# Performance work log

Hardware: AMD Instinct MI355X
Metric: run time of the kernel (lower is better)

Reference implementation:

```python
import jax, jax.numpy as jnp
import numpy as np

N_NODES = 100000


def gcn_conv(x, W, b, src, dst, n_nodes):
    # Linear transform first (PyG GCNConv applies weight before propagation)
    h = x @ W  # [N, out]
    # gcn_norm with self-loops: deg[i] = 1 + #incoming edges at i
    ones = jnp.ones(src.shape[0], dtype=h.dtype)
    deg = jax.ops.segment_sum(ones, dst, num_segments=n_nodes) + 1.0
    dinv = jax.lax.rsqrt(deg)  # deg^{-1/2}, deg >= 1 so safe
    norm = dinv[src] * dinv[dst]  # [E]
    # aggregate normalized messages at destination nodes
    agg = jax.ops.segment_sum(h[src] * norm[:, None], dst, num_segments=n_nodes)
    # self-loop contribution: norm_ii = dinv[i]^2
    agg = agg + h * (dinv * dinv)[:, None]
    return agg + b


def setup_inputs() -> dict:
    key = jax.random.key(0)
    k1, k2, k3, k4, k5, k6 = jax.random.split(key, 6)
    num_features, hidden, num_classes = 512, 128, 64
    x = jax.random.normal(k1, (N_NODES, num_features), dtype=jnp.float32)
    edge_index = jax.random.randint(k2, (2, 1600000), 0, N_NODES, dtype=jnp.int64)
    # Glorot-style params (scaled normals)
    W1 = jax.random.normal(k3, (num_features, hidden), dtype=jnp.float32) / np.sqrt(num_features)
    b1 = jnp.zeros((hidden,), dtype=jnp.float32)
    W2 = jax.random.normal(k4, (hidden, num_classes), dtype=jnp.float32) / np.sqrt(hidden)
    b2 = jnp.zeros((num_classes,), dtype=jnp.float32)
    return {"x": x, "edge_index": edge_index, "W1": W1, "b1": b1, "W2": W2, "b2": b2}


def reference(x, edge_index, W1, b1, W2, b2):
    src, dst = edge_index[0], edge_index[1]
    h = jax.nn.relu(gcn_conv(x, W1, b1, src, dst, N_NODES))
    out = gcn_conv(h, W2, b2, src, dst, N_NODES)
    return jax.nn.log_softmax(out, axis=1)
```

## Files before the change

### kernel.cpp

```cpp
#include <hip/hip_runtime.h>
#include <cmath>

#define N_NODES 100000
#define N_EDGES 1600000
#define F_IN 512
#define F_HID 128
#define F_OUT 64

#define SCAN_NB ((N_NODES + 255) / 256)

#define BK_SHIFT 10
#define NBUK ((N_NODES + 1023) >> 10)
#define SCAP 24576
#define LSLOT 64
#define NBLK_A 512
#define FILL_SPLIT 8
#define NPS (1024 / FILL_SPLIT)
#define OV_CAP 4096

typedef __attribute__((ext_vector_type(8))) short short8;
typedef __attribute__((ext_vector_type(4))) float float4v;

#define GLOAD_LDS16(g, l)                                                      \
    __builtin_amdgcn_global_load_lds(                                          \
        (const __attribute__((address_space(1))) void*)(g),                    \
        (__attribute__((address_space(3))) void*)(l), 16, 0, 0)

__device__ __forceinline__ unsigned short f2bf(float f) {
    unsigned u = __builtin_bit_cast(unsigned, f);
    u += 0x7FFFu + ((u >> 16) & 1u);
    return (unsigned short)(u >> 16);
}
__device__ __forceinline__ float bf2f(unsigned short s) {
    unsigned u = ((unsigned)s) << 16;
    return __builtin_bit_cast(float, u);
}
__device__ __forceinline__ float lo_bf(unsigned u) {
    return __builtin_bit_cast(float, u << 16);
}
__device__ __forceinline__ float hi_bf(unsigned u) {
    return __builtin_bit_cast(float, u & 0xFFFF0000u);
}
__device__ __forceinline__ short8 cvt8(float4 lo, float4 hi) {
    return short8{(short)f2bf(lo.x), (short)f2bf(lo.y), (short)f2bf(lo.z), (short)f2bf(lo.w),
                  (short)f2bf(hi.x), (short)f2bf(hi.y), (short)f2bf(hi.z), (short)f2bf(hi.w)};
}
__device__ __forceinline__ unsigned pack_bf2(float a, float b) {
    return (unsigned)f2bf(a) | ((unsigned)f2bf(b) << 16);
}

template <int N>
__device__ __forceinline__ void waitvm() {
    if constexpr (N == 0) asm volatile("s_waitcnt vmcnt(0)" ::: "memory");
    else if constexpr (N == 3) asm volatile("s_waitcnt vmcnt(3)" ::: "memory");
    else if constexpr (N == 6) asm volatile("s_waitcnt vmcnt(6)" ::: "memory");
    else static_assert(N == 0 || N == 3 || N == 6, "add literal");
}
#define LGKM0() asm volatile("s_waitcnt lgkmcnt(0)" ::: "memory")
#define BAR() __builtin_amdgcn_s_barrier()
#define SCHED0() __builtin_amdgcn_sched_barrier(0)

__global__ __launch_bounds__(256) void partition_kernel(
    const int* __restrict__ src, const int* __restrict__ dst,
    int* __restrict__ deg, unsigned* __restrict__ staging, int* __restrict__ gcur,
    unsigned long long* __restrict__ ovbuf, int* __restrict__ ovcnt) {
    __shared__ unsigned buf[NBUK][LSLOT];
    __shared__ int cnt[NBUK];
    int tid = threadIdx.x;
    for (int b = tid; b < NBUK; b += 256) cnt[b] = 0;
    __syncthreads();
    constexpr int PER = (((N_EDGES + NBLK_A - 1) / NBLK_A) + 3) & ~3;
    int e0 = blockIdx.x * PER;
    int e1 = min(e0 + PER, N_EDGES);

    auto body = [&](int d, int s) {
        atomicAdd(&deg[d], 1);
        int b = d >> BK_SHIFT;
        unsigned rec = (unsigned)s | ((unsigned)(d & 1023) << 17);
        int slot = atomicAdd(&cnt[b], 1);
        if (slot < LSLOT) {
            buf[b][slot] = rec;
        } else {
            int op = atomicAdd(ovcnt, 1);
            if (op < OV_CAP)
                ovbuf[op] = ((unsigned long long)(unsigned)d << 32) | (unsigned)s;
        }
    };
    auto drain = [&](void) {
        for (int b = tid; b < NBUK; b += 256) {
            int c = min(cnt[b], LSLOT);
            int full = c & ~15;
            if (full > 0) {
                int pos = atomicAdd(&gcur[b], full);
                if (pos + full <= SCAP) {
                    unsigned* dp = &staging[(size_t)b * SCAP + pos];
                    for (int i = 0; i < full; ++i) dp[i] = buf[b][i];
                }
                for (int i = 0; i < c - full; ++i) buf[b][i] = buf[b][full + i];
            }
            cnt[b] = c - full;
        }
    };

    int base = e0;
    for (; base + 1024 <= e1; base += 1024) {
        int e = base + tid * 4;
        int4 dv = *(const int4*)(dst + e);
        int4 sv = *(const int4*)(src + e);
        body(dv.x, sv.x);
        body(dv.y, sv.y);
        body(dv.z, sv.z);
        body(dv.w, sv.w);
        __syncthreads();
        drain();
        __syncthreads();
    }
    for (int e = base + tid; e < e1; e += 256) body(dst[e], src[e]);
    __syncthreads();
    drain();
    __syncthreads();
    for (int b = tid; b < NBUK; b += 256) {
        int c = cnt[b];
        if (c > 0) {
            int pos = atomicAdd(&gcur[b], c);
            if (pos + c <= SCAP)
                for (int i = 0; i < c; ++i) staging[(size_t)b * SCAP + pos + i] = buf[b][i];
        }
    }
}

__global__ __launch_bounds__(256) void fill_kernel(
    const unsigned* __restrict__ staging, const int* __restrict__ gcur,
    const int* __restrict__ row_ptr, int* __restrict__ csr_src,
    const unsigned long long* __restrict__ ovbuf, const int* __restrict__ ovcnt) {
    int b = blockIdx.x / FILL_SPLIT;
    int slice = blockIdx.x - b * FILL_SPLIT;
    int dl0 = slice * NPS;
    int node0 = (b << BK_SHIFT) + dl0;
    __shared__ int lcur[NPS];
    int tid = threadIdx.x;
    if (tid < NPS) {
        int nd = node0 + tid;
        lcur[tid] = (nd < N_NODES) ? row_ptr[nd] : 0;
    }
    __syncthreads();

    int n = gcur[b];
    if (n > SCAP) n = SCAP;
    const unsigned* sp = &staging[(size_t)b * SCAP];

    auto process = [&](unsigned rec) {
        int dl = (int)(rec >> 17) - dl0;
        if ((unsigned)dl < (unsigned)NPS) {
            int pos = atomicAdd(&lcur[dl], 1);
            csr_src[pos] = (int)(rec & 0x1FFFFu);
        }
    };

    int i = tid * 4;
    for (; i + 4 <= n; i += 1024) {
        uint4 r = *(const uint4*)(sp + i);
        process(r.x);
        process(r.y);
        process(r.z);
        process(r.w);
    }
    int tail0 = n & ~3;
    if (tid < (n - tail0)) process(sp[tail0 + tid]);

    int oc = *ovcnt;
    if (oc > OV_CAP) oc = OV_CAP;
    for (int k = tid; k < oc; k += 256) {
        unsigned long long r = ovbuf[k];
        int d = (int)(r >> 32);
        int dl = d - node0;
        if ((d >> BK_SHIFT) == b && (unsigned)dl < (unsigned)NPS) {
            int pos = atomicAdd(&lcur[dl], 1);
            csr_src[pos] = (int)(r & 0xffffffffu);
        }
    }
}


__global__ __launch_bounds__(256) void block_sum_kernel(const int* __restrict__ deg,
                                                        int* __restrict__ bsum, int n) {
    int g = blockIdx.x * 256 + threadIdx.x;
    int v = (g < n) ? deg[g] : 0;
    __shared__ int ws[4];
    int lane = threadIdx.x & 63;
    int w = threadIdx.x >> 6;
#pragma unroll
    for (int o = 32; o > 0; o >>= 1) v += __shfl_down(v, o, 64);
    if (lane == 0) ws[w] = v;
    __syncthreads();
    if (threadIdx.x == 0) bsum[blockIdx.x] = ws[0] + ws[1] + ws[2] + ws[3];
}

__global__ __launch_bounds__(512) void scan_partials_kernel(int* __restrict__ bsum, int nb) {
    __shared__ int t[512];
    int tid = threadIdx.x;
    int v = (tid < nb) ? bsum[tid] : 0;
    t[tid] = v;
    __syncthreads();
    for (int d = 1; d < 512; d <<= 1) {
        int u = (tid >= d) ? t[tid - d] : 0;
        __syncthreads();
        t[tid] += u;
        __syncthreads();
    }
    if (tid < nb) bsum[tid] = t[tid] - v;
}

__global__ __launch_bounds__(256) void scan_final_kernel(const int* __restrict__ deg,
                                                         const int* __restrict__ bsum,
                                                         int* __restrict__ row_ptr,
                                                         float* __restrict__ dinv, int n) {
    __shared__ int t[256];
    int g = blockIdx.x * 256 + threadIdx.x;
    int tid = threadIdx.x;
    int v = (g < n) ? deg[g] : 0;
    t[tid] = v;
    __syncthreads();
    for (int d = 1; d < 256; d <<= 1) {
        int u = (tid >= d) ? t[tid - d] : 0;
        __syncthreads();
        t[tid] += u;
        __syncthreads();
    }
    int off = bsum[blockIdx.x] + t[tid] - v;
    if (g < n) {
        row_ptr[g] = off;
        dinv[g] = rsqrtf((float)(v + 1));
    }
    if (g == n - 1) row_ptr[n] = off + v;
}


__global__ void transpose_w_kernel(const float* __restrict__ W1, const float* __restrict__ W2,
                                   unsigned short* __restrict__ Wt1,
                                   unsigned short* __restrict__ Wt2) {
    int g = blockIdx.x * 256 + threadIdx.x;
    if (g < F_HID * F_IN) {
        int n = g >> 9, k = g & 511;
        Wt1[g] = f2bf(W1[k * F_HID + n]);
    } else {
        int h = g - F_HID * F_IN;
        if (h < F_OUT * F_HID) {
            int n = h >> 7, k = h & 127;
            Wt2[h] = f2bf(W2[k * F_OUT + n]);
        }
    }
}


template <int BN, int K, bool A_BF16>
__global__ __launch_bounds__(256, 3) void gemm_lds_kernel(
    const void* __restrict__ Araw, const unsigned short* __restrict__ Wt,
    const float* __restrict__ dinv, unsigned short* __restrict__ out, int N) {
    constexpr int NCT = BN / 16;
    constexpr int AE = A_BF16 ? 2 : 4;
    constexpr int SLOTS_A = (32 * AE) / 16;
    constexpr int MA = SLOTS_A - 1;
    constexpr int ABYTES = 128 * 32 * AE;
    constexpr int BBYTES = BN * 32 * 2;
    constexpr int NT = K / 32;
    constexpr int SL = (128 * SLOTS_A + BN * 4) / 256;

    __shared__ __align__(128) char Abuf[2][ABYTES];
    __shared__ __align__(128) char Bbuf[2][BBYTES];

    const char* Ab = (const char*)Araw;
    const char* Bb = (const char*)Wt;
    int tid = threadIdx.x;
    int lane = tid & 63;
    int wv = tid >> 6;
    int row0 = blockIdx.x * 128;
    int l15 = lane & 15;
    int q = lane >> 4;

    float4v acc[2][NCT] = {};

    auto stage = [&](int buf, int k0) {
        constexpr int CA = 128 * SLOTS_A;
#pragma unroll
        for (int i = 0; i < CA / 256; ++i) {
            int c = i * 256 + tid;
            int cw = i * 256 + (tid & ~63);
            int row = c / SLOTS_A;
            int s = c & MA;
            int g = s ^ (row & MA);
            int rg = row0 + row;
            if (rg >= N) rg = N - 1;
            GLOAD_LDS16(Ab + ((size_t)rg * K + k0) * AE + g * 16,
                        &Abuf[buf][cw * 16]);
        }
        constexpr int CB = BN * 4;
#pragma unroll
        for (int i = 0; i < CB / 256; ++i) {
            int c = i * 256 + tid;
            int cw = i * 256 + (tid & ~63);
            int col = c >> 2;
            int s = c & 3;
            int g = s ^ (col & 3);
            GLOAD_LDS16(Bb + ((size_t)col * K + k0) * 2 + g * 16,
                        &Bbuf[buf][cw * 16]);
        }
    };

    auto compute = [&](int buf) {
        const char* Ac = Abuf[buf];
        const char* Bc = Bbuf[buf];
        int lr0 = wv * 32 + l15;
        int lr1 = lr0 + 16;
        short8 a0, a1;
        if constexpr (A_BF16) {
            int s0 = q ^ (lr0 & 3);
            int s1 = q ^ (lr1 & 3);
            a0 = *(const short8*)(Ac + lr0 * 64 + s0 * 16);
            a1 = *(const short8*)(Ac + lr1 * 64 + s1 * 16);
        } else {
            int r7a = lr0 & 7, r7b = lr1 & 7;
            float4 f0 = *(const float4*)(Ac + lr0 * 128 + ((2 * q) ^ r7a) * 16);
            float4 f1 = *(const float4*)(Ac + lr0 * 128 + ((2 * q + 1) ^ r7a) * 16);
            float4 f2 = *(const float4*)(Ac + lr1 * 128 + ((2 * q) ^ r7b) * 16);
            float4 f3 = *(const float4*)(Ac + lr1 * 128 + ((2 * q + 1) ^ r7b) * 16);
            a0 = cvt8(f0, f1);
            a1 = cvt8(f2, f3);
        }
#pragma unroll
        for (int ct = 0; ct < NCT; ++ct) {
            int col = ct * 16 + l15;
            int sb = q ^ (col & 3);
            short8 b = *(const short8*)(Bc + col * 64 + sb * 16);
            acc[0][ct] = __builtin_amdgcn_mfma_f32_16x16x32_bf16(a0, b, acc[0][ct], 0, 0, 0);
            acc[1][ct] = __builtin_amdgcn_mfma_f32_16x16x32_bf16(a1, b, acc[1][ct], 0, 0, 0);
        }
    };

    stage(0, 0);
    stage(1, 32);
#pragma unroll 1
    for (int t = 0; t < NT - 2; ++t) {
        waitvm<SL>();
        BAR();
        SCHED0();
        compute(t & 1);
        LGKM0();
        BAR();
        SCHED0();
        stage(t & 1, (t + 2) * 32);
    }
    waitvm<SL>();
    BAR();
    SCHED0();
    compute((NT - 2) & 1);
    waitvm<0>();
    BAR();
    SCHED0();
    compute((NT - 1) & 1);

#pragma unroll
    for (int rt = 0; rt < 2; ++rt) {
#pragma unroll
        for (int reg = 0; reg < 4; ++reg) {
            int row = row0 + wv * 32 + rt * 16 + q * 4 + reg;
            if (row < N) {
                float sc = dinv[row];
#pragma unroll
                for (int ct = 0; ct < NCT; ++ct) {
                    out[(size_t)row * BN + ct * 16 + l15] = f2bf(acc[rt][ct][reg] * sc);
                }
            }
        }
    }
}


__global__ __launch_bounds__(256) void agg1_kernel(
    const uint2* __restrict__ g1v, const int* __restrict__ row_ptr,
    const int* __restrict__ csr_src, const float* __restrict__ dinv,
    const float4* __restrict__ b1v, uint2* __restrict__ h1v) {
    int tid = threadIdx.x;
    int wv = tid >> 6;
    int lane = tid & 63;
    int half = lane >> 5;
    int hl = lane & 31;
    int node = blockIdx.x * 8 + wv * 2 + half;
    uint2 u = g1v[(size_t)node * 32 + hl];
    float a0 = lo_bf(u.x), a1 = hi_bf(u.x), a2 = lo_bf(u.y), a3 = hi_bf(u.y);
    int e = row_ptr[node], end = row_ptr[node + 1];
    for (; e + 8 <= end; e += 8) {
        int j0 = csr_src[e + 0], j1 = csr_src[e + 1], j2 = csr_src[e + 2], j3 = csr_src[e + 3];
        int j4 = csr_src[e + 4], j5 = csr_src[e + 5], j6 = csr_src[e + 6], j7 = csr_src[e + 7];
        uint2 v0 = g1v[(size_t)j0 * 32 + hl];
        uint2 v1 = g1v[(size_t)j1 * 32 + hl];
        uint2 v2 = g1v[(size_t)j2 * 32 + hl];
        uint2 v3 = g1v[(size_t)j3 * 32 + hl];
        uint2 v4 = g1v[(size_t)j4 * 32 + hl];
        uint2 v5 = g1v[(size_t)j5 * 32 + hl];
        uint2 v6 = g1v[(size_t)j6 * 32 + hl];
        uint2 v7 = g1v[(size_t)j7 * 32 + hl];
        a0 += ((lo_bf(v0.x) + lo_bf(v1.x)) + (lo_bf(v2.x) + lo_bf(v3.x))) +
              ((lo_bf(v4.x) + lo_bf(v5.x)) + (lo_bf(v6.x) + lo_bf(v7.x)));
        a1 += ((hi_bf(v0.x) + hi_bf(v1.x)) + (hi_bf(v2.x) + hi_bf(v3.x))) +
              ((hi_bf(v4.x) + hi_bf(v5.x)) + (hi_bf(v6.x) + hi_bf(v7.x)));
        a2 += ((lo_bf(v0.y) + lo_bf(v1.y)) + (lo_bf(v2.y) + lo_bf(v3.y))) +
              ((lo_bf(v4.y) + lo_bf(v5.y)) + (lo_bf(v6.y) + lo_bf(v7.y)));
        a3 += ((hi_bf(v0.y) + hi_bf(v1.y)) + (hi_bf(v2.y) + hi_bf(v3.y))) +
              ((hi_bf(v4.y) + hi_bf(v5.y)) + (hi_bf(v6.y) + hi_bf(v7.y)));
    }
    for (; e + 2 <= end; e += 2) {
        int j0 = csr_src[e + 0], j1 = csr_src[e + 1];
        uint2 v0 = g1v[(size_t)j0 * 32 + hl];
        uint2 v1 = g1v[(size_t)j1 * 32 + hl];
        a0 += lo_bf(v0.x) + lo_bf(v1.x);
        a1 += hi_bf(v0.x) + hi_bf(v1.x);
        a2 += lo_bf(v0.y) + lo_bf(v1.y);
        a3 += hi_bf(v0.y) + hi_bf(v1.y);
    }
    for (; e < end; ++e) {
        uint2 v0 = g1v[(size_t)csr_src[e] * 32 + hl];
        a0 += lo_bf(v0.x);
        a1 += hi_bf(v0.x);
        a2 += lo_bf(v0.y);
        a3 += hi_bf(v0.y);
    }
    float d = dinv[node];
    float4 b = b1v[hl];
    float r0 = fmaxf(d * a0 + b.x, 0.0f);
    float r1 = fmaxf(d * a1 + b.y, 0.0f);
    float r2 = fmaxf(d * a2 + b.z, 0.0f);
    float r3 = fmaxf(d * a3 + b.w, 0.0f);
    h1v[(size_t)node * 32 + hl] = uint2{pack_bf2(r0, r1), pack_bf2(r2, r3)};
}

__global__ __launch_bounds__(256) void agg2_lsm_kernel(
    const unsigned* __restrict__ g2v, const int* __restrict__ row_ptr,
    const int* __restrict__ csr_src, const float* __restrict__ dinv,
    const float2* __restrict__ b2v, float2* __restrict__ outv) {
    int tid = threadIdx.x;
    int wv = tid >> 6;
    int lane = tid & 63;
    int half = lane >> 5;
    int hl = lane & 31;
    int node = blockIdx.x * 8 + wv * 2 + half;
    unsigned u = g2v[(size_t)node * 32 + hl];
    float a0 = lo_bf(u), a1 = hi_bf(u);
    int e = row_ptr[node], end = row_ptr[node + 1];
    for (; e + 8 <= end; e += 8) {
        int j0 = csr_src[e + 0], j1 = csr_src[e + 1], j2 = csr_src[e + 2], j3 = csr_src[e + 3];
        int j4 = csr_src[e + 4], j5 = csr_src[e + 5], j6 = csr_src[e + 6], j7 = csr_src[e + 7];
        unsigned v0 = g2v[(size_t)j0 * 32 + hl];
        unsigned v1 = g2v[(size_t)j1 * 32 + hl];
        unsigned v2 = g2v[(size_t)j2 * 32 + hl];
        unsigned v3 = g2v[(size_t)j3 * 32 + hl];
        unsigned v4 = g2v[(size_t)j4 * 32 + hl];
        unsigned v5 = g2v[(size_t)j5 * 32 + hl];
        unsigned v6 = g2v[(size_t)j6 * 32 + hl];
        unsigned v7 = g2v[(size_t)j7 * 32 + hl];
        a0 += ((lo_bf(v0) + lo_bf(v1)) + (lo_bf(v2) + lo_bf(v3))) +
              ((lo_bf(v4) + lo_bf(v5)) + (lo_bf(v6) + lo_bf(v7)));
        a1 += ((hi_bf(v0) + hi_bf(v1)) + (hi_bf(v2) + hi_bf(v3))) +
              ((hi_bf(v4) + hi_bf(v5)) + (hi_bf(v6) + hi_bf(v7)));
    }
    for (; e + 2 <= end; e += 2) {
        unsigned v0 = g2v[(size_t)csr_src[e + 0] * 32 + hl];
        unsigned v1 = g2v[(size_t)csr_src[e + 1] * 32 + hl];
        a0 += lo_bf(v0) + lo_bf(v1);
        a1 += hi_bf(v0) + hi_bf(v1);
    }
    for (; e < end; ++e) {
        unsigned v0 = g2v[(size_t)csr_src[e] * 32 + hl];
        a0 += lo_bf(v0);
        a1 += hi_bf(v0);
    }
    float d = dinv[node];
    float2 b = b2v[hl];
    float v0 = d * a0 + b.x;
    float v1 = d * a1 + b.y;
    float m = fmaxf(v0, v1);
#pragma unroll
    for (int o = 16; o > 0; o >>= 1) m = fmaxf(m, __shfl_xor(m, o, 64));
    float s = __expf(v0 - m) + __expf(v1 - m);
#pragma unroll
    for (int o = 16; o > 0; o >>= 1) s += __shfl_xor(s, o, 64);
    float ls = __logf(s);
    outv[(size_t)node * 32 + hl] = float2{v0 - m - ls, v1 - m - ls};
}


extern "C" void kernel_launch(void* const* d_in, const int* in_sizes, int n_in,
                              void* d_out, int out_size, void* d_ws, size_t ws_size,
                              hipStream_t stream) {
    const float* x  = (const float*)d_in[0];
    const int* eidx = (const int*)d_in[1];
    const float* W1 = (const float*)d_in[2];
    const float* b1 = (const float*)d_in[3];
    const float* W2 = (const float*)d_in[4];
    const float* b2 = (const float*)d_in[5];
    float* out = (float*)d_out;
    const int* src = eidx;
    const int* dst = eidx + N_EDGES;

    char* base = (char*)d_ws;
    size_t off = 0;
    auto alloc = [&](size_t bytes) -> void* {
        void* p = base + off;
        off += (bytes + 255) & ~(size_t)255;
        return p;
    };
    int* zbase    = (int*)alloc((size_t)(N_NODES + NBUK + 64) * 4);
    int* deg      = zbase;
    int* gcur     = zbase + N_NODES;
    int* ovcnt    = zbase + N_NODES + NBUK;
    int* row_ptr  = (int*)alloc((size_t)(N_NODES + 1) * 4);
    float* dinv   = (float*)alloc((size_t)N_NODES * 4);
    int* bsum     = (int*)alloc((size_t)SCAN_NB * 4);
    unsigned* staging = (unsigned*)alloc((size_t)NBUK * SCAP * 4);
    unsigned long long* ovbuf = (unsigned long long*)alloc((size_t)OV_CAP * 8);
    int* csr_src  = (int*)alloc((size_t)N_EDGES * 4);
    unsigned short* Wt1 = (unsigned short*)alloc((size_t)F_HID * F_IN * 2);
    unsigned short* Wt2 = (unsigned short*)alloc((size_t)F_OUT * F_HID * 2);
    unsigned short* g1  = (unsigned short*)alloc((size_t)N_NODES * F_HID * 2);
    unsigned short* h1  = (unsigned short*)alloc((size_t)N_NODES * F_HID * 2);
    unsigned short* g2  = g1;

    hipMemsetAsync(zbase, 0, (size_t)(N_NODES + NBUK + 64) * 4, stream);
    partition_kernel<<<NBLK_A, 256, 0, stream>>>(src, dst, deg, staging, gcur, ovbuf, ovcnt);
    block_sum_kernel<<<SCAN_NB, 256, 0, stream>>>(deg, bsum, N_NODES);
    scan_partials_kernel<<<1, 512, 0, stream>>>(bsum, SCAN_NB);
    scan_final_kernel<<<SCAN_NB, 256, 0, stream>>>(deg, bsum, row_ptr, dinv, N_NODES);
    fill_kernel<<<NBUK * FILL_SPLIT, 256, 0, stream>>>(staging, gcur, row_ptr, csr_src, ovbuf, ovcnt);
    transpose_w_kernel<<<(F_HID * F_IN + F_OUT * F_HID + 255) / 256, 256, 0, stream>>>(
        W1, W2, Wt1, Wt2);

    int gblocks = (N_NODES + 127) / 128;
    gemm_lds_kernel<F_HID, F_IN, false><<<gblocks, 256, 0, stream>>>(
        (const void*)x, Wt1, dinv, g1, N_NODES);
    agg1_kernel<<<N_NODES / 8, 256, 0, stream>>>(
        (const uint2*)g1, row_ptr, csr_src, dinv, (const float4*)b1, (uint2*)h1);

    gemm_lds_kernel<F_OUT, F_HID, true><<<gblocks, 256, 0, stream>>>(
        (const void*)h1, Wt2, dinv, g2, N_NODES);
    agg2_lsm_kernel<<<N_NODES / 8, 256, 0, stream>>>(
        (const unsigned*)g2, row_ptr, csr_src, dinv, (const float2*)b2, (float2*)out);
}
```

Before: 557.5 us.

## Compute degrees via per-bucket LDS histogram and widen aggregation gathers to 16B

Removes the global atomicAdd on deg for every edge in the partition kernel. Degrees are now computed by a new per-bucket kernel that builds an LDS histogram from the staged records and the overflow buffer. Both aggregation kernels now use quarter-wave groups (16 lanes per node) with wider vector loads, uint4 for layer 1 and uint2 for layer 2, so each gather issues fewer, larger memory transactions and the log-softmax reduction needs fewer shuffles. This adds one kernel launch and an extra pass over the staging buffer, and each lane now holds more accumulators.

```diff
diff --git a/kernel.cpp b/kernel.cpp
--- a/kernel.cpp
+++ b/kernel.cpp
@@ -62,7 +62,7 @@
 
 __global__ __launch_bounds__(256) void partition_kernel(
     const int* __restrict__ src, const int* __restrict__ dst,
-    int* __restrict__ deg, unsigned* __restrict__ staging, int* __restrict__ gcur,
+    unsigned* __restrict__ staging, int* __restrict__ gcur,
     unsigned long long* __restrict__ ovbuf, int* __restrict__ ovcnt) {
     __shared__ unsigned buf[NBUK][LSLOT];
     __shared__ int cnt[NBUK];
@@ -74,7 +74,6 @@
     int e1 = min(e0 + PER, N_EDGES);
 
     auto body = [&](int d, int s) {
-        atomicAdd(&deg[d], 1);
         int b = d >> BK_SHIFT;
         unsigned rec = (unsigned)s | ((unsigned)(d & 1023) << 17);
         int slot = atomicAdd(&cnt[b], 1);
@@ -126,6 +125,42 @@
             if (pos + c <= SCAP)
                 for (int i = 0; i < c; ++i) staging[(size_t)b * SCAP + pos + i] = buf[b][i];
         }
+    }
+}
+
+__global__ __launch_bounds__(256) void deg_hist_kernel(
+    const unsigned* __restrict__ staging, const int* __restrict__ gcur,
+    const unsigned long long* __restrict__ ovbuf, const int* __restrict__ ovcnt,
+    int* __restrict__ deg) {
+    int b = blockIdx.x;
+    __shared__ int hist[1024];
+    int tid = threadIdx.x;
+    for (int i = tid; i < 1024; i += 256) hist[i] = 0;
+    __syncthreads();
+    int n = gcur[b];
+    if (n > SCAP) n = SCAP;
+    const unsigned* sp = &staging[(size_t)b * SCAP];
+    int i = tid * 4;
+    for (; i + 4 <= n; i += 1024) {
+        uint4 r = *(const uint4*)(sp + i);
+        atomicAdd(&hist[r.x >> 17], 1);
+        atomicAdd(&hist[r.y >> 17], 1);
+        atomicAdd(&hist[r.z >> 17], 1);
+        atomicAdd(&hist[r.w >> 17], 1);
+    }
+    int tail0 = n & ~3;
+    if (tid < (n - tail0)) atomicAdd(&hist[sp[tail0 + tid] >> 17], 1);
+    int oc = *ovcnt;
+    if (oc > OV_CAP) oc = OV_CAP;
+    for (int k = tid; k < oc; k += 256) {
+        int d = (int)(ovbuf[k] >> 32);
+        if ((d >> BK_SHIFT) == b) atomicAdd(&hist[d & 1023], 1);
+    }
+    __syncthreads();
+    int node0 = b << BK_SHIFT;
+    for (int j = tid; j < 1024; j += 256) {
+        int nd = node0 + j;
+        if (nd < N_NODES) deg[nd] = hist[j];
     }
 }
 
@@ -377,115 +412,109 @@
 
 
 __global__ __launch_bounds__(256) void agg1_kernel(
-    const uint2* __restrict__ g1v, const int* __restrict__ row_ptr,
+    const uint4* __restrict__ g1v, const int* __restrict__ row_ptr,
     const int* __restrict__ csr_src, const float* __restrict__ dinv,
-    const float4* __restrict__ b1v, uint2* __restrict__ h1v) {
+    const float4* __restrict__ b1v, uint4* __restrict__ h1v) {
     int tid = threadIdx.x;
     int wv = tid >> 6;
     int lane = tid & 63;
-    int half = lane >> 5;
-    int hl = lane & 31;
-    int node = blockIdx.x * 8 + wv * 2 + half;
-    uint2 u = g1v[(size_t)node * 32 + hl];
+    int qt = lane >> 4;
+    int ql = lane & 15;
+    int node = blockIdx.x * 16 + wv * 4 + qt;
+    uint4 u = g1v[(size_t)node * 16 + ql];
     float a0 = lo_bf(u.x), a1 = hi_bf(u.x), a2 = lo_bf(u.y), a3 = hi_bf(u.y);
+    float a4 = lo_bf(u.z), a5 = hi_bf(u.z), a6 = lo_bf(u.w), a7 = hi_bf(u.w);
     int e = row_ptr[node], end = row_ptr[node + 1];
+#define ACC8(v)                                                                \
+    a0 += lo_bf(v.x); a1 += hi_bf(v.x); a2 += lo_bf(v.y); a3 += hi_bf(v.y);    \
+    a4 += lo_bf(v.z); a5 += hi_bf(v.z); a6 += lo_bf(v.w); a7 += hi_bf(v.w)
     for (; e + 8 <= end; e += 8) {
         int j0 = csr_src[e + 0], j1 = csr_src[e + 1], j2 = csr_src[e + 2], j3 = csr_src[e + 3];
         int j4 = csr_src[e + 4], j5 = csr_src[e + 5], j6 = csr_src[e + 6], j7 = csr_src[e + 7];
-        uint2 v0 = g1v[(size_t)j0 * 32 + hl];
-        uint2 v1 = g1v[(size_t)j1 * 32 + hl];
-        uint2 v2 = g1v[(size_t)j2 * 32 + hl];
-        uint2 v3 = g1v[(size_t)j3 * 32 + hl];
-        uint2 v4 = g1v[(size_t)j4 * 32 + hl];
-        uint2 v5 = g1v[(size_t)j5 * 32 + hl];
-        uint2 v6 = g1v[(size_t)j6 * 32 + hl];
-        uint2 v7 = g1v[(size_t)j7 * 32 + hl];
-        a0 += ((lo_bf(v0.x) + lo_bf(v1.x)) + (lo_bf(v2.x) + lo_bf(v3.x))) +
-              ((lo_bf(v4.x) + lo_bf(v5.x)) + (lo_bf(v6.x) + lo_bf(v7.x)));
-        a1 += ((hi_bf(v0.x) + hi_bf(v1.x)) + (hi_bf(v2.x) + hi_bf(v3.x))) +
-              ((hi_bf(v4.x) + hi_bf(v5.x)) + (hi_bf(v6.x) + hi_bf(v7.x)));
-        a2 += ((lo_bf(v0.y) + lo_bf(v1.y)) + (lo_bf(v2.y) + lo_bf(v3.y))) +
-              ((lo_bf(v4.y) + lo_bf(v5.y)) + (lo_bf(v6.y) + lo_bf(v7.y)));
-        a3 += ((hi_bf(v0.y) + hi_bf(v1.y)) + (hi_bf(v2.y) + hi_bf(v3.y))) +
-              ((hi_bf(v4.y) + hi_bf(v5.y)) + (hi_bf(v6.y) + hi_bf(v7.y)));
+        uint4 v0 = g1v[(size_t)j0 * 16 + ql];
+        uint4 v1 = g1v[(size_t)j1 * 16 + ql];
+        uint4 v2 = g1v[(size_t)j2 * 16 + ql];
+        uint4 v3 = g1v[(size_t)j3 * 16 + ql];
+        uint4 v4 = g1v[(size_t)j4 * 16 + ql];
+        uint4 v5 = g1v[(size_t)j5 * 16 + ql];
+        uint4 v6 = g1v[(size_t)j6 * 16 + ql];
+        uint4 v7 = g1v[(size_t)j7 * 16 + ql];
+        ACC8(v0); ACC8(v1); ACC8(v2); ACC8(v3);
+        ACC8(v4); ACC8(v5); ACC8(v6); ACC8(v7);
     }
     for (; e + 2 <= end; e += 2) {
-        int j0 = csr_src[e + 0], j1 = csr_src[e + 1];
-        uint2 v0 = g1v[(size_t)j0 * 32 + hl];
-        uint2 v1 = g1v[(size_t)j1 * 32 + hl];
-        a0 += lo_bf(v0.x) + lo_bf(v1.x);
-        a1 += hi_bf(v0.x) + hi_bf(v1.x);
-        a2 += lo_bf(v0.y) + lo_bf(v1.y);
-        a3 += hi_bf(v0.y) + hi_bf(v1.y);
+        uint4 v0 = g1v[(size_t)csr_src[e + 0] * 16 + ql];
+        uint4 v1 = g1v[(size_t)csr_src[e + 1] * 16 + ql];
+        ACC8(v0); ACC8(v1);
     }
     for (; e < end; ++e) {
-        uint2 v0 = g1v[(size_t)csr_src[e] * 32 + hl];
-        a0 += lo_bf(v0.x);
-        a1 += hi_bf(v0.x);
-        a2 += lo_bf(v0.y);
-        a3 += hi_bf(v0.y);
-    }
+        uint4 v0 = g1v[(size_t)csr_src[e] * 16 + ql];
+        ACC8(v0);
+    }
+#undef ACC8
     float d = dinv[node];
-    float4 b = b1v[hl];
-    float r0 = fmaxf(d * a0 + b.x, 0.0f);
-    float r1 = fmaxf(d * a1 + b.y, 0.0f);
-    float r2 = fmaxf(d * a2 + b.z, 0.0f);
-    float r3 = fmaxf(d * a3 + b.w, 0.0f);
-    h1v[(size_t)node * 32 + hl] = uint2{pack_bf2(r0, r1), pack_bf2(r2, r3)};
+    float4 ba = b1v[2 * ql], bb = b1v[2 * ql + 1];
+    float r0 = fmaxf(d * a0 + ba.x, 0.0f), r1 = fmaxf(d * a1 + ba.y, 0.0f);
+    float r2 = fmaxf(d * a2 + ba.z, 0.0f), r3 = fmaxf(d * a3 + ba.w, 0.0f);
+    float r4 = fmaxf(d * a4 + bb.x, 0.0f), r5 = fmaxf(d * a5 + bb.y, 0.0f);
+    float r6 = fmaxf(d * a6 + bb.z, 0.0f), r7 = fmaxf(d * a7 + bb.w, 0.0f);
+    h1v[(size_t)node * 16 + ql] =
+        uint4{pack_bf2(r0, r1), pack_bf2(r2, r3), pack_bf2(r4, r5), pack_bf2(r6, r7)};
 }
 
 __global__ __launch_bounds__(256) void agg2_lsm_kernel(
-    const unsigned* __restrict__ g2v, const int* __restrict__ row_ptr,
+    const uint2* __restrict__ g2v, const int* __restrict__ row_ptr,
     const int* __restrict__ csr_src, const float* __restrict__ dinv,
-    const float2* __restrict__ b2v, float2* __restrict__ outv) {
+    const float4* __restrict__ b2v, float4* __restrict__ outv) {
     int tid = threadIdx.x;
     int wv = tid >> 6;
     int lane = tid & 63;
-    int half = lane >> 5;
-    int hl = lane & 31;
-    int node = blockIdx.x * 8 + wv * 2 + half;
-    unsigned u = g2v[(size_t)node * 32 + hl];
-    float a0 = lo_bf(u), a1 = hi_bf(u);
+    int qt = lane >> 4;
+    int ql = lane & 15;
+    int node = blockIdx.x * 16 + wv * 4 + qt;
+    uint2 u = g2v[(size_t)node * 16 + ql];
+    float a0 = lo_bf(u.x), a1 = hi_bf(u.x), a2 = lo_bf(u.y), a3 = hi_bf(u.y);
     int e = row_ptr[node], end = row_ptr[node + 1];
+#define ACC4(v)                                                                \
+    a0 += lo_bf(v.x); a1 += hi_bf(v.x); a2 += lo_bf(v.y); a3 += hi_bf(v.y)
     for (; e + 8 <= end; e += 8) {
         int j0 = csr_src[e + 0], j1 = csr_src[e + 1], j2 = csr_src[e + 2], j3 = csr_src[e + 3];
         int j4 = csr_src[e + 4], j5 = csr_src[e + 5], j6 = csr_src[e + 6], j7 = csr_src[e + 7];
-        unsigned v0 = g2v[(size_t)j0 * 32 + hl];
-        unsigned v1 = g2v[(size_t)j1 * 32 + hl];
-        unsigned v2 = g2v[(size_t)j2 * 32 + hl];
-        unsigned v3 = g2v[(size_t)j3 * 32 + hl];
-        unsigned v4 = g2v[(size_t)j4 * 32 + hl];
-        unsigned v5 = g2v[(size_t)j5 * 32 + hl];
-        unsigned v6 = g2v[(size_t)j6 * 32 + hl];
-        unsigned v7 = g2v[(size_t)j7 * 32 + hl];
-        a0 += ((lo_bf(v0) + lo_bf(v1)) + (lo_bf(v2) + lo_bf(v3))) +
-              ((lo_bf(v4) + lo_bf(v5)) + (lo_bf(v6) + lo_bf(v7)));
-        a1 += ((hi_bf(v0) + hi_bf(v1)) + (hi_bf(v2) + hi_bf(v3))) +
-              ((hi_bf(v4) + hi_bf(v5)) + (hi_bf(v6) + hi_bf(v7)));
+        uint2 v0 = g2v[(size_t)j0 * 16 + ql];
+        uint2 v1 = g2v[(size_t)j1 * 16 + ql];
+        uint2 v2 = g2v[(size_t)j2 * 16 + ql];
+        uint2 v3 = g2v[(size_t)j3 * 16 + ql];
+        uint2 v4 = g2v[(size_t)j4 * 16 + ql];
+        uint2 v5 = g2v[(size_t)j5 * 16 + ql];
+        uint2 v6 = g2v[(size_t)j6 * 16 + ql];
+        uint2 v7 = g2v[(size_t)j7 * 16 + ql];
+        ACC4(v0); ACC4(v1); ACC4(v2); ACC4(v3);
+        ACC4(v4); ACC4(v5); ACC4(v6); ACC4(v7);
     }
     for (; e + 2 <= end; e += 2) {
-        unsigned v0 = g2v[(size_t)csr_src[e + 0] * 32 + hl];
-        unsigned v1 = g2v[(size_t)csr_src[e + 1] * 32 + hl];
-        a0 += lo_bf(v0) + lo_bf(v1);
-        a1 += hi_bf(v0) + hi_bf(v1);
+        uint2 v0 = g2v[(size_t)csr_src[e + 0] * 16 + ql];
+        uint2 v1 = g2v[(size_t)csr_src[e + 1] * 16 + ql];
+        ACC4(v0); ACC4(v1);
     }
     for (; e < end; ++e) {
-        unsigned v0 = g2v[(size_t)csr_src[e] * 32 + hl];
-        a0 += lo_bf(v0);
-        a1 += hi_bf(v0);
-    }
+        uint2 v0 = g2v[(size_t)csr_src[e] * 16 + ql];
+        ACC4(v0);
+    }
+#undef ACC4
     float d = dinv[node];
-    float2 b = b2v[hl];
+    float4 b = b2v[ql];
     float v0 = d * a0 + b.x;
     float v1 = d * a1 + b.y;
-    float m = fmaxf(v0, v1);
-#pragma unroll
-    for (int o = 16; o > 0; o >>= 1) m = fmaxf(m, __shfl_xor(m, o, 64));
-    float s = __expf(v0 - m) + __expf(v1 - m);
-#pragma unroll
-    for (int o = 16; o > 0; o >>= 1) s += __shfl_xor(s, o, 64);
-    float ls = __logf(s);
-    outv[(size_t)node * 32 + hl] = float2{v0 - m - ls, v1 - m - ls};
+    float v2 = d * a2 + b.z;
+    float v3 = d * a3 + b.w;
+    float m = fmaxf(fmaxf(v0, v1), fmaxf(v2, v3));
+#pragma unroll
+    for (int o = 8; o > 0; o >>= 1) m = fmaxf(m, __shfl_xor(m, o, 64));
+    float s = __expf(v0 - m) + __expf(v1 - m) + __expf(v2 - m) + __expf(v3 - m);
+#pragma unroll
+    for (int o = 8; o > 0; o >>= 1) s += __shfl_xor(s, o, 64);
+    float ls = m + __logf(s);
+    outv[(size_t)node * 16 + ql] = float4{v0 - ls, v1 - ls, v2 - ls, v3 - ls};
 }
 
 
@@ -509,10 +538,10 @@
         off += (bytes + 255) & ~(size_t)255;
         return p;
     };
-    int* zbase    = (int*)alloc((size_t)(N_NODES + NBUK + 64) * 4);
-    int* deg      = zbase;
-    int* gcur     = zbase + N_NODES;
-    int* ovcnt    = zbase + N_NODES + NBUK;
+    int* zbase    = (int*)alloc((size_t)(NBUK + 64) * 4);
+    int* gcur     = zbase;
+    int* ovcnt    = zbase + NBUK;
+    int* deg      = (int*)alloc((size_t)N_NODES * 4);
     int* row_ptr  = (int*)alloc((size_t)(N_NODES + 1) * 4);
     float* dinv   = (float*)alloc((size_t)N_NODES * 4);
     int* bsum     = (int*)alloc((size_t)SCAN_NB * 4);
@@ -525,8 +554,9 @@
     unsigned short* h1  = (unsigned short*)alloc((size_t)N_NODES * F_HID * 2);
     unsigned short* g2  = g1;
 
-    hipMemsetAsync(zbase, 0, (size_t)(N_NODES + NBUK + 64) * 4, stream);
-    partition_kernel<<<NBLK_A, 256, 0, stream>>>(src, dst, deg, staging, gcur, ovbuf, ovcnt);
+    hipMemsetAsync(zbase, 0, (size_t)(NBUK + 64) * 4, stream);
+    partition_kernel<<<NBLK_A, 256, 0, stream>>>(src, dst, staging, gcur, ovbuf, ovcnt);
+    deg_hist_kernel<<<NBUK, 256, 0, stream>>>(staging, gcur, ovbuf, ovcnt, deg);
     block_sum_kernel<<<SCAN_NB, 256, 0, stream>>>(deg, bsum, N_NODES);
     scan_partials_kernel<<<1, 512, 0, stream>>>(bsum, SCAN_NB);
     scan_final_kernel<<<SCAN_NB, 256, 0, stream>>>(deg, bsum, row_ptr, dinv, N_NODES);
@@ -537,11 +567,11 @@
     int gblocks = (N_NODES + 127) / 128;
     gemm_lds_kernel<F_HID, F_IN, false><<<gblocks, 256, 0, stream>>>(
         (const void*)x, Wt1, dinv, g1, N_NODES);
-    agg1_kernel<<<N_NODES / 8, 256, 0, stream>>>(
-        (const uint2*)g1, row_ptr, csr_src, dinv, (const float4*)b1, (uint2*)h1);
+    agg1_kernel<<<N_NODES / 16, 256, 0, stream>>>(
+        (const uint4*)g1, row_ptr, csr_src, dinv, (const float4*)b1, (uint4*)h1);
 
     gemm_lds_kernel<F_OUT, F_HID, true><<<gblocks, 256, 0, stream>>>(
         (const void*)h1, Wt2, dinv, g2, N_NODES);
-    agg2_lsm_kernel<<<N_NODES / 8, 256, 0, stream>>>(
-        (const unsigned*)g2, row_ptr, csr_src, dinv, (const float2*)b2, (float2*)out);
-}
+    agg2_lsm_kernel<<<N_NODES / 16, 256, 0, stream>>>(
+        (const uint2*)g2, row_ptr, csr_src, dinv, (const float4*)b2, (float4*)out);
+}
```

Result: faster. 500.9 us (-10.2%).
